# Performance work log

Measured on AMD Instinct MI355X. Metric: run time of the kernel, lower is better.

Reference implementation:

```python
import jax, jax.numpy as jnp
import numpy as np
import math

B, S, D = 4, 2048, 1024
WINDOW = 10  # window_size; attends to |i-j| <= WINDOW//2


def setup_inputs() -> dict:
    key = jax.random.key(0)
    ks = jax.random.split(key, 9)
    sc = 1.0 / math.sqrt(D)
    return {
        "x": jax.random.normal(ks[0], (B, S, D), dtype=jnp.float32),
        "Wq": jax.random.normal(ks[1], (D, D), dtype=jnp.float32) * sc,
        "bq": jnp.zeros((D,), dtype=jnp.float32),
        "Wk": jax.random.normal(ks[2], (D, D), dtype=jnp.float32) * sc,
        "bk": jnp.zeros((D,), dtype=jnp.float32),
        "Wv": jax.random.normal(ks[3], (D, D), dtype=jnp.float32) * sc,
        "bv": jnp.zeros((D,), dtype=jnp.float32),
        "Wo": jax.random.normal(ks[4], (D, D), dtype=jnp.float32) * sc,
        "bo": jnp.zeros((D,), dtype=jnp.float32),
    }


def _local_mask(seq_len: int, window_size: int) -> jnp.ndarray:
    # row i attends to columns [i - w//2, i + w//2] inclusive -> |i - j| <= w//2
    i = jnp.arange(seq_len)[:, None]
    j = jnp.arange(seq_len)[None, :]
    return jnp.abs(i - j) <= (window_size // 2)  # [S, S] bool


def reference(x, Wq, bq, Wk, bk, Wv, bv, Wo, bo):
    # nn.Linear: y = x @ W.T + b
    Q = x @ Wq.T + bq  # [B, S, D]
    K = x @ Wk.T + bk
    V = x @ Wv.T + bv
    scores = jnp.einsum("bqd,bkd->bqk", Q, K) / jnp.float32(math.sqrt(D))
    mask = _local_mask(x.shape[1], WINDOW)
    scores = jnp.where(mask[None, :, :], scores, jnp.float32(-1e9))
    attn = jax.nn.softmax(scores, axis=-1)  # [B, S, S]
    context = jnp.einsum("bqk,bkd->bqd", attn, V)
    output = context @ Wo.T + bo
    return output, attn
```

## Files before the change

### kernel.cpp

```cpp
#include <hip/hip_runtime.h>
#include <hip/hip_bf16.h>
#include <cstdint>
#include <cstddef>


typedef __attribute__((ext_vector_type(8))) short bf16x8;
typedef __attribute__((ext_vector_type(4))) float f32x4;
typedef __attribute__((ext_vector_type(8))) unsigned short ushortx8;

#define GPTR(x) ((const __attribute__((address_space(1))) void*)(x))
#define LPTR(x) ((__attribute__((address_space(3))) void*)(x))

__device__ __forceinline__ unsigned short f2bf(float f) {
    __hip_bfloat16 h = __float2bfloat16(f);
    unsigned short u;
    __builtin_memcpy(&u, &h, 2);
    return u;
}
__device__ __forceinline__ float bf2f(unsigned short u) {
    unsigned int x = ((unsigned int)u) << 16;
    float f;
    __builtin_memcpy(&f, &x, 4);
    return f;
}

__global__ void cvt_all(const float* __restrict__ x,
                        const float* __restrict__ Wq, const float* __restrict__ Wk,
                        const float* __restrict__ Wv, const float* __restrict__ Wo,
                        unsigned short* __restrict__ xh,
                        unsigned short* __restrict__ Wcat,
                        unsigned short* __restrict__ Woh) {
    const int idx = blockIdx.x * blockDim.x + threadIdx.x;
    const float* src;
    unsigned short* dst;
    int s_off, d_off;
    if (idx < 2097152) {
        src = x; dst = xh; s_off = idx; d_off = idx;
    } else {
        const int r   = idx - 2097152;
        const int seg = r >> 18;
        const int off = r & 262143;
        src   = (seg == 0) ? Wq : (seg == 1) ? Wk : (seg == 2) ? Wv : Wo;
        dst   = (seg < 3) ? Wcat : Woh;
        s_off = off;
        d_off = (seg < 3) ? (seg << 18) + off : off;
    }
    f32x4 v = reinterpret_cast<const f32x4*>(src)[s_off];
    ushort4 o;
    o.x = f2bf(v[0]); o.y = f2bf(v[1]); o.z = f2bf(v[2]); o.w = f2bf(v[3]);
    reinterpret_cast<ushort4*>(dst)[d_off] = o;
}


__device__ __forceinline__ void stage_half(const char* gtile, size_t rstride,
                                           size_t k0b, unsigned short* ltile,
                                           int h1, int w, int lane) {
    const int r0   = (w << 4) + (lane >> 3);
    const int colb = (lane & 7) << 4;
#pragma unroll
    for (int q = 0; q < 2; ++q) {
        const int rt   = h1 * 128 + r0 + q * 8;
        const int csrc = colb ^ ((rt & 7) << 4);
        __builtin_amdgcn_global_load_lds(
            GPTR(gtile + (size_t)rt * rstride + k0b + (size_t)csrc),
            LPTR((char*)ltile + (size_t)(h1 * 16384 + w * 2048 + q * 1024)),
            16, 0, 0);
    }
}

__launch_bounds__(512, 2)
__global__ void gemm_qkv_8ph(const unsigned short* __restrict__ A,
                             const unsigned short* __restrict__ Bw,
                             const float* __restrict__ bq,
                             const float* __restrict__ bk,
                             const float* __restrict__ bv,
                             unsigned short* __restrict__ C,
                             int M, int N, int K) {
    __shared__ unsigned short As[2][256 * 64];
    __shared__ unsigned short Bs[2][256 * 64];

    const int tid  = threadIdx.x;
    const int lane = tid & 63;
    const int w    = tid >> 6;
    const int wr   = w >> 2;
    const int wc   = w & 3;

    const int nb    = gridDim.x;
    const int chunk = nb >> 3;
    const int sid   = (blockIdx.x & 7) * chunk + (blockIdx.x >> 3);
    const int ntn   = N >> 8;
    const int tm    = sid / ntn;
    const int tn    = sid % ntn;

    f32x4 acc[8][4];
#pragma unroll
    for (int m = 0; m < 8; ++m)
#pragma unroll
        for (int n = 0; n < 4; ++n) acc[m][n] = (f32x4){0.f, 0.f, 0.f, 0.f};

    const size_t rstride = (size_t)K * 2;
    const char* Ag = (const char*)(A + (size_t)tm * 256 * (size_t)K);
    const char* Bg = (const char*)(Bw + (size_t)tn * 256 * (size_t)K);

#pragma unroll
    for (int h = 0; h < 4; ++h)
        stage_half(h < 2 ? Ag : Bg, rstride, 0,
                   h < 2 ? As[0] : Bs[0], h & 1, w, lane);
    __syncthreads();

    const int NT = K >> 6;
    unsigned short* Acur = As[0]; unsigned short* Bcur = Bs[0];
    unsigned short* Anxt = As[1]; unsigned short* Bnxt = Bs[1];

    const int swz = (lane & 7) << 4;
    const int cb0 = (lane >> 4) << 4;

    for (int t = 0; t < NT; ++t) {
        if (t + 1 < NT) {
            const size_t k0b = (size_t)(t + 1) << 7;
#pragma unroll
            for (int h = 0; h < 4; ++h)
                stage_half(h < 2 ? Ag : Bg, rstride, k0b,
                           h < 2 ? Anxt : Bnxt, h & 1, w, lane);
        }
#pragma unroll
        for (int kk = 0; kk < 2; ++kk) {
            bf16x8 b[4];
#pragma unroll
            for (int n = 0; n < 4; ++n) {
                const int row = wc * 64 + n * 16 + (lane & 15);
                b[n] = *reinterpret_cast<const bf16x8*>(
                    (const char*)Bcur + row * 128 + ((kk * 64 + cb0) ^ swz));
            }
#pragma unroll
            for (int mh = 0; mh < 2; ++mh) {
                bf16x8 a[4];
#pragma unroll
                for (int m = 0; m < 4; ++m) {
                    const int row = wr * 128 + mh * 64 + m * 16 + (lane & 15);
                    a[m] = *reinterpret_cast<const bf16x8*>(
                        (const char*)Acur + row * 128 + ((kk * 64 + cb0) ^ swz));
                }
                __builtin_amdgcn_s_setprio(1);
#pragma unroll
                for (int m = 0; m < 4; ++m)
#pragma unroll
                    for (int n = 0; n < 4; ++n)
                        acc[mh * 4 + m][n] = __builtin_amdgcn_mfma_f32_16x16x32_bf16(
                            a[m], b[n], acc[mh * 4 + m][n], 0, 0, 0);
                __builtin_amdgcn_s_setprio(0);
                if (kk != 1 || mh != 1)
                    __builtin_amdgcn_s_barrier();
            }
        }
        __syncthreads();
        unsigned short* ta = Acur; Acur = Anxt; Anxt = ta;
        unsigned short* tb = Bcur; Bcur = Bnxt; Bnxt = tb;
    }

    const int col0 = tn * 256 + wc * 64 + (lane & 15);
    const int row0 = tm * 256 + wr * 128 + ((lane >> 4) << 2);
#pragma unroll
    for (int n = 0; n < 4; ++n) {
        const int col = col0 + n * 16;
        const int seg = col >> 10;
        const float bb = (seg == 0 ? bq : seg == 1 ? bk : bv)[col & 1023];
#pragma unroll
        for (int m = 0; m < 8; ++m) {
            const int row = row0 + m * 16;
#pragma unroll
            for (int r = 0; r < 4; ++r)
                C[(size_t)(row + r) * (size_t)N + col] = f2bf(acc[m][n][r] + bb);
        }
    }
}

__device__ __forceinline__ void gemm_core(const unsigned short* __restrict__ A,
                                          const unsigned short* __restrict__ Bw,
                                          int K, int tm, int tn,
                                          unsigned short* As, unsigned short* Bs,
                                          f32x4 (&acc)[4][4]) {
    const int tid  = threadIdx.x;
    const int lane = tid & 63;
    const int w    = tid >> 6;
    const int wr   = w >> 1;
    const int wc   = w & 1;

    const int lrow8 = lane >> 3;
    const int lcolb = (lane & 7) << 4;

    const char* Abase = (const char*)(A + (size_t)tm * 128 * (size_t)K);
    const char* Bbase = (const char*)(Bw + (size_t)tn * 128 * (size_t)K);
    const size_t rstride = (size_t)K * 2;

    const int nk = K >> 6;
    for (int t = 0; t < nk; ++t) {
        const size_t k0b = ((size_t)t << 6) * 2;
#pragma unroll
        for (int ii = 0; ii < 4; ++ii) {
            const int c    = (w << 2) + ii;
            const int row  = (c << 3) + lrow8;
            const int csrc = lcolb ^ ((row & 7) << 4);
            __builtin_amdgcn_global_load_lds(
                GPTR(Abase + (size_t)row * rstride + k0b + (size_t)csrc),
                LPTR((char*)As + (c << 10)), 16, 0, 0);
            __builtin_amdgcn_global_load_lds(
                GPTR(Bbase + (size_t)row * rstride + k0b + (size_t)csrc),
                LPTR((char*)Bs + (c << 10)), 16, 0, 0);
        }
        __syncthreads();

#pragma unroll
        for (int kk = 0; kk < 2; ++kk) {
            bf16x8 af[4], bfr[4];
            const int cb = (kk << 6) + ((lane >> 4) << 4);
#pragma unroll
            for (int m = 0; m < 4; ++m) {
                const int row = (wr << 6) + (m << 4) + (lane & 15);
                af[m] = *reinterpret_cast<const bf16x8*>(
                    (const char*)As + row * 128 + (cb ^ ((row & 7) << 4)));
            }
#pragma unroll
            for (int n = 0; n < 4; ++n) {
                const int row = (wc << 6) + (n << 4) + (lane & 15);
                bfr[n] = *reinterpret_cast<const bf16x8*>(
                    (const char*)Bs + row * 128 + (cb ^ ((row & 7) << 4)));
            }
#pragma unroll
            for (int m = 0; m < 4; ++m)
#pragma unroll
                for (int n = 0; n < 4; ++n)
                    acc[m][n] = __builtin_amdgcn_mfma_f32_16x16x32_bf16(
                        af[m], bfr[n], acc[m][n], 0, 0, 0);
        }
        __syncthreads();
    }
}

__launch_bounds__(256, 2)
__global__ void gemm_out(const unsigned short* __restrict__ A,
                         const unsigned short* __restrict__ Bw,
                         const float* __restrict__ bias,
                         float* __restrict__ C, int M, int N, int K) {
    __shared__ unsigned short As[128 * 64];
    __shared__ unsigned short Bs[128 * 64];
    f32x4 acc[4][4];
#pragma unroll
    for (int m = 0; m < 4; ++m)
#pragma unroll
        for (int n = 0; n < 4; ++n) acc[m][n] = (f32x4){0.f, 0.f, 0.f, 0.f};

    gemm_core(A, Bw, K, blockIdx.x, blockIdx.y, As, Bs, acc);

    const int lane = threadIdx.x & 63;
    const int w    = threadIdx.x >> 6;
    const int wr   = w >> 1, wc = w & 1;
    const int col0 = (blockIdx.y << 7) + (wc << 6) + (lane & 15);
    const int row0 = (blockIdx.x << 7) + (wr << 6) + ((lane >> 4) << 2);
#pragma unroll
    for (int n = 0; n < 4; ++n) {
        const int col = col0 + (n << 4);
        const float bb = bias[col];
#pragma unroll
        for (int m = 0; m < 4; ++m) {
            const int row = row0 + (m << 4);
#pragma unroll
            for (int r = 0; r < 4; ++r)
                C[(size_t)(row + r) * (size_t)N + col] = acc[m][n][r] + bb;
        }
    }
}

__launch_bounds__(256, 4)
__global__ void attn_band_kernel(const unsigned short* __restrict__ QKV,
                                 float* __restrict__ attn,
                                 unsigned short* __restrict__ ctx) {
    __shared__ float psm[4][16];
    const int bid  = blockIdx.x;
    const int rb   = (bid & 7) * 256 + (bid >> 3);
    const int w    = threadIdx.x >> 6;
    const int lane = threadIdx.x & 63;
    const int g    = (rb << 2) + w;
    const int b    = g >> 11;
    const int i    = g & 2047;

    const unsigned short* qrow = QKV + (size_t)g * 3072;
    float qf[16];
    {
        ushortx8 qa = *reinterpret_cast<const ushortx8*>(qrow + (lane << 4));
        ushortx8 qb = *reinterpret_cast<const ushortx8*>(qrow + (lane << 4) + 8);
#pragma unroll
        for (int t = 0; t < 8; ++t) { qf[t] = bf2f(qa[t]); qf[8 + t] = bf2f(qb[t]); }
    }

    float s[11];
#pragma unroll
    for (int jj = 0; jj < 11; ++jj) {
        const int j = i - 5 + jj;
        const bool valid = ((unsigned)j < 2048u);
        const int jc = min(max(j, 0), 2047);
        const unsigned short* krow = QKV + ((size_t)(b << 11) + jc) * 3072 + 1024;
        ushortx8 ka = *reinterpret_cast<const ushortx8*>(krow + (lane << 4));
        ushortx8 kb = *reinterpret_cast<const ushortx8*>(krow + (lane << 4) + 8);
        float d = 0.f;
#pragma unroll
        for (int t = 0; t < 8; ++t)
            d += qf[t] * bf2f(ka[t]) + qf[8 + t] * bf2f(kb[t]);
#pragma unroll
        for (int off = 32; off >= 1; off >>= 1) d += __shfl_xor(d, off, 64);
        s[jj] = valid ? d * 0.03125f : -1e30f;
    }

    float mx = s[0];
#pragma unroll
    for (int jj = 1; jj < 11; ++jj) mx = fmaxf(mx, s[jj]);
    float p[11], sum = 0.f;
#pragma unroll
    for (int jj = 0; jj < 11; ++jj) { p[jj] = expf(s[jj] - mx); sum += p[jj]; }
    const float inv = 1.0f / sum;

    if (lane == 0) {
#pragma unroll
        for (int jj = 0; jj < 11; ++jj) psm[w][jj] = p[jj] * inv;
    }
    __syncthreads();

    const int lo = i - 5;
    float* arow = attn + (size_t)g * 2048;
#pragma unroll
    for (int e = 0; e < 8; ++e) {
        const int c0 = (e << 8) + (lane << 2);
        f32x4 v = (f32x4){0.f, 0.f, 0.f, 0.f};
        if (c0 + 3 >= lo && c0 <= lo + 10) {
#pragma unroll
            for (int t = 0; t < 4; ++t) {
                const int d = c0 + t - lo;
                if ((unsigned)d < 11u) v[t] = psm[w][d];
            }
        }
        *reinterpret_cast<f32x4*>(arow + c0) = v;
    }

    float cacc[16];
#pragma unroll
    for (int t = 0; t < 16; ++t) cacc[t] = 0.f;
#pragma unroll
    for (int jj = 0; jj < 11; ++jj) {
        const int j  = i - 5 + jj;
        const int jc = min(max(j, 0), 2047);
        const float pj = p[jj] * inv;
        const unsigned short* vrow = QKV + ((size_t)(b << 11) + jc) * 3072 + 2048;
        ushortx8 va = *reinterpret_cast<const ushortx8*>(vrow + (lane << 4));
        ushortx8 vb = *reinterpret_cast<const ushortx8*>(vrow + (lane << 4) + 8);
#pragma unroll
        for (int t = 0; t < 8; ++t) {
            cacc[t]     += pj * bf2f(va[t]);
            cacc[8 + t] += pj * bf2f(vb[t]);
        }
    }
    unsigned short* cp = ctx + (size_t)g * 1024 + (lane << 4);
    ushortx8 oa, ob;
#pragma unroll
    for (int t = 0; t < 8; ++t) { oa[t] = f2bf(cacc[t]); ob[t] = f2bf(cacc[8 + t]); }
    *reinterpret_cast<ushortx8*>(cp)     = oa;
    *reinterpret_cast<ushortx8*>(cp + 8) = ob;
}

extern "C" void kernel_launch(void* const* d_in, const int* in_sizes, int n_in,
                              void* d_out, int out_size, void* d_ws, size_t ws_size,
                              hipStream_t stream) {
    const float* x  = (const float*)d_in[0];
    const float* Wq = (const float*)d_in[1];
    const float* bq = (const float*)d_in[2];
    const float* Wk = (const float*)d_in[3];
    const float* bk = (const float*)d_in[4];
    const float* Wv = (const float*)d_in[5];
    const float* bv = (const float*)d_in[6];
    const float* Wo = (const float*)d_in[7];
    const float* bo = (const float*)d_in[8];

    const size_t MS = 8192, DD = 1024;

    float* out  = (float*)d_out;
    float* attn = out + MS * DD;

    char* ws = (char*)d_ws;
    unsigned short* xh   = (unsigned short*)ws; ws += MS * DD * 2;
    unsigned short* Wcat = (unsigned short*)ws; ws += 3 * DD * DD * 2;
    unsigned short* Woh  = (unsigned short*)ws; ws += DD * DD * 2;
    unsigned short* QKV  = (unsigned short*)ws; ws += MS * 3 * DD * 2;
    unsigned short* ctx  = (unsigned short*)ws; ws += MS * DD * 2;

    cvt_all<<<dim3(12288), dim3(256), 0, stream>>>(x, Wq, Wk, Wv, Wo, xh, Wcat, Woh);

    gemm_qkv_8ph<<<dim3(384), dim3(512), 0, stream>>>(xh, Wcat, bq, bk, bv,
                                                      QKV, 8192, 3072, 1024);

    attn_band_kernel<<<dim3(2048), dim3(256), 0, stream>>>(QKV, attn, ctx);

    gemm_out<<<dim3(64, 8), dim3(256), 0, stream>>>(ctx, Woh, bo, out, 8192, 1024, 1024);
}
```

Measured before the change: 144.5 us.

## Split QKV GEMM tiles into k-half units with finer-grained async staging

Restructures the QKV projection GEMM's LDS layout into per-k-half units with a new XOR swizzle. It replaces the full-tile double buffer plus __syncthreads with staged loads issued between MFMA phases, synchronised by vmcnt waits and s_barrier. The aim is to overlap global-to-LDS copies with compute more finely and remove the full-block sync per k-step. The risk is that the manual vmcnt counting is fragile and could race, or could stall if the count is wrong.

New measurement: 165.0 us. +14.2%, slower.

```diff
diff --git a/kernel.cpp b/kernel.cpp
--- a/kernel.cpp
+++ b/kernel.cpp
@@ -52,20 +52,24 @@
 }
 
 
-__device__ __forceinline__ void stage_half(const char* gtile, size_t rstride,
-                                           size_t k0b, unsigned short* ltile,
-                                           int h1, int w, int lane) {
-    const int r0   = (w << 4) + (lane >> 3);
-    const int colb = (lane & 7) << 4;
+__device__ __forceinline__ void stage_unit(const char* gtile, size_t rstride,
+                                           size_t kbyte, unsigned short* unit,
+                                           int w, int lane) {
 #pragma unroll
     for (int q = 0; q < 2; ++q) {
-        const int rt   = h1 * 128 + r0 + q * 8;
-        const int csrc = colb ^ ((rt & 7) << 4);
+        const int s0  = (w << 7) + (q << 6) + lane;
+        const int row = s0 >> 2;
+        const int c   = (s0 & 3) ^ ((s0 >> 4) & 3);
         __builtin_amdgcn_global_load_lds(
-            GPTR(gtile + (size_t)rt * rstride + k0b + (size_t)csrc),
-            LPTR((char*)ltile + (size_t)(h1 * 16384 + w * 2048 + q * 1024)),
+            GPTR(gtile + (size_t)row * rstride + kbyte + (size_t)(c << 4)),
+            LPTR((char*)unit + ((w << 11) + (q << 10))),
             16, 0, 0);
     }
+}
+
+__device__ __forceinline__ bf16x8 frag(const unsigned short* unit, int row, int cs) {
+    const int slot = (row << 2) + ((cs ^ (row >> 2)) & 3);
+    return *reinterpret_cast<const bf16x8*>((const char*)unit + (slot << 4));
 }
 
 __launch_bounds__(512, 2)
@@ -76,14 +80,16 @@
                              const float* __restrict__ bv,
                              unsigned short* __restrict__ C,
                              int M, int N, int K) {
-    __shared__ unsigned short As[2][256 * 64];
-    __shared__ unsigned short Bs[2][256 * 64];
+    __shared__ unsigned short As[2][2][8192];
+    __shared__ unsigned short Bs[2][2][8192];
 
     const int tid  = threadIdx.x;
     const int lane = tid & 63;
     const int w    = tid >> 6;
     const int wr   = w >> 2;
     const int wc   = w & 3;
+    const int l15  = lane & 15;
+    const int cs   = lane >> 4;
 
     const int nb    = gridDim.x;
     const int chunk = nb >> 3;
@@ -102,64 +108,90 @@
     const char* Ag = (const char*)(A + (size_t)tm * 256 * (size_t)K);
     const char* Bg = (const char*)(Bw + (size_t)tn * 256 * (size_t)K);
 
-#pragma unroll
-    for (int h = 0; h < 4; ++h)
-        stage_half(h < 2 ? Ag : Bg, rstride, 0,
-                   h < 2 ? As[0] : Bs[0], h & 1, w, lane);
-    __syncthreads();
+    stage_unit(Ag, rstride, 0,  As[0][0], w, lane);
+    stage_unit(Bg, rstride, 0,  Bs[0][0], w, lane);
+    stage_unit(Ag, rstride, 64, As[0][1], w, lane);
+    stage_unit(Bg, rstride, 64, Bs[0][1], w, lane);
 
     const int NT = K >> 6;
-    unsigned short* Acur = As[0]; unsigned short* Bcur = Bs[0];
-    unsigned short* Anxt = As[1]; unsigned short* Bnxt = Bs[1];
-
-    const int swz = (lane & 7) << 4;
-    const int cb0 = (lane >> 4) << 4;
+    int buf = 0;
 
     for (int t = 0; t < NT; ++t) {
-        if (t + 1 < NT) {
-            const size_t k0b = (size_t)(t + 1) << 7;
-#pragma unroll
-            for (int h = 0; h < 4; ++h)
-                stage_half(h < 2 ? Ag : Bg, rstride, k0b,
-                           h < 2 ? Anxt : Bnxt, h & 1, w, lane);
-        }
-#pragma unroll
-        for (int kk = 0; kk < 2; ++kk) {
-            bf16x8 b[4];
-#pragma unroll
-            for (int n = 0; n < 4; ++n) {
-                const int row = wc * 64 + n * 16 + (lane & 15);
-                b[n] = *reinterpret_cast<const bf16x8*>(
-                    (const char*)Bcur + row * 128 + ((kk * 64 + cb0) ^ swz));
-            }
-#pragma unroll
-            for (int mh = 0; mh < 2; ++mh) {
-                bf16x8 a[4];
-#pragma unroll
-                for (int m = 0; m < 4; ++m) {
-                    const int row = wr * 128 + mh * 64 + m * 16 + (lane & 15);
-                    a[m] = *reinterpret_cast<const bf16x8*>(
-                        (const char*)Acur + row * 128 + ((kk * 64 + cb0) ^ swz));
-                }
-                __builtin_amdgcn_s_setprio(1);
-#pragma unroll
-                for (int m = 0; m < 4; ++m)
-#pragma unroll
-                    for (int n = 0; n < 4; ++n)
-                        acc[mh * 4 + m][n] = __builtin_amdgcn_mfma_f32_16x16x32_bf16(
-                            a[m], b[n], acc[mh * 4 + m][n], 0, 0, 0);
-                __builtin_amdgcn_s_setprio(0);
-                if (kk != 1 || mh != 1)
-                    __builtin_amdgcn_s_barrier();
-            }
-        }
-        __syncthreads();
-        unsigned short* ta = Acur; Acur = Anxt; Anxt = ta;
-        unsigned short* tb = Bcur; Bcur = Bnxt; Bnxt = tb;
-    }
-
-    const int col0 = tn * 256 + wc * 64 + (lane & 15);
-    const int row0 = tm * 256 + wr * 128 + ((lane >> 4) << 2);
+        const bool sv = (t + 1 < NT);
+        const unsigned short* A0 = As[buf][0];
+        const unsigned short* A1 = As[buf][1];
+        const unsigned short* B0 = Bs[buf][0];
+        const unsigned short* B1 = Bs[buf][1];
+        unsigned short* nA0 = As[buf ^ 1][0];
+        unsigned short* nA1 = As[buf ^ 1][1];
+        unsigned short* nB0 = Bs[buf ^ 1][0];
+        unsigned short* nB1 = Bs[buf ^ 1][1];
+        const size_t kb = (size_t)(t + 1) << 7;
+
+        bf16x8 a[4], b[4];
+
+        asm volatile("s_waitcnt vmcnt(4)" ::: "memory");
+        __builtin_amdgcn_s_barrier();
+        if (sv) stage_unit(Ag, rstride, kb, nA0, w, lane);
+#pragma unroll
+        for (int n = 0; n < 4; ++n) b[n] = frag(B0, wc * 64 + n * 16 + l15, cs);
+#pragma unroll
+        for (int m = 0; m < 4; ++m) a[m] = frag(A0, wr * 128 + m * 16 + l15, cs);
+        __builtin_amdgcn_s_setprio(1);
+#pragma unroll
+        for (int m = 0; m < 4; ++m)
+#pragma unroll
+            for (int n = 0; n < 4; ++n)
+                acc[m][n] = __builtin_amdgcn_mfma_f32_16x16x32_bf16(
+                    a[m], b[n], acc[m][n], 0, 0, 0);
+        __builtin_amdgcn_s_setprio(0);
+
+        if (sv) stage_unit(Bg, rstride, kb, nB0, w, lane);
+#pragma unroll
+        for (int m = 0; m < 4; ++m) a[m] = frag(A0, wr * 128 + 64 + m * 16 + l15, cs);
+        __builtin_amdgcn_s_setprio(1);
+#pragma unroll
+        for (int m = 0; m < 4; ++m)
+#pragma unroll
+            for (int n = 0; n < 4; ++n)
+                acc[4 + m][n] = __builtin_amdgcn_mfma_f32_16x16x32_bf16(
+                    a[m], b[n], acc[4 + m][n], 0, 0, 0);
+        __builtin_amdgcn_s_setprio(0);
+
+        if (sv) { asm volatile("s_waitcnt vmcnt(4)" ::: "memory"); }
+        else    { asm volatile("s_waitcnt vmcnt(0)" ::: "memory"); }
+        __builtin_amdgcn_s_barrier();
+        if (sv) stage_unit(Ag, rstride, kb + 64, nA1, w, lane);
+#pragma unroll
+        for (int n = 0; n < 4; ++n) b[n] = frag(B1, wc * 64 + n * 16 + l15, cs);
+#pragma unroll
+        for (int m = 0; m < 4; ++m) a[m] = frag(A1, wr * 128 + m * 16 + l15, cs);
+        __builtin_amdgcn_s_setprio(1);
+#pragma unroll
+        for (int m = 0; m < 4; ++m)
+#pragma unroll
+            for (int n = 0; n < 4; ++n)
+                acc[m][n] = __builtin_amdgcn_mfma_f32_16x16x32_bf16(
+                    a[m], b[n], acc[m][n], 0, 0, 0);
+        __builtin_amdgcn_s_setprio(0);
+
+        if (sv) stage_unit(Bg, rstride, kb + 64, nB1, w, lane);
+#pragma unroll
+        for (int m = 0; m < 4; ++m) a[m] = frag(A1, wr * 128 + 64 + m * 16 + l15, cs);
+        __builtin_amdgcn_s_setprio(1);
+#pragma unroll
+        for (int m = 0; m < 4; ++m)
+#pragma unroll
+            for (int n = 0; n < 4; ++n)
+                acc[4 + m][n] = __builtin_amdgcn_mfma_f32_16x16x32_bf16(
+                    a[m], b[n], acc[4 + m][n], 0, 0, 0);
+        __builtin_amdgcn_s_setprio(0);
+
+        buf ^= 1;
+    }
+
+    const int col0 = tn * 256 + wc * 64 + l15;
+    const int row0 = tm * 256 + wr * 128 + (cs << 2);
 #pragma unroll
     for (int n = 0; n < 4; ++n) {
         const int col = col0 + n * 16;
```
